# Kernel optimization log

Hardware: AMD Instinct MI355X
Metric: run time of the kernel (lower is better)

The kernel has to match this reference:

```python
import jax, jax.numpy as jnp
import numpy as np

B, V, H, W = 8, 2, 1024, 1024
N = 131072
TH_MIN, TH_MAX = 0.0, 500.0
ALPHA = 0.5


def _make_extrinsics():
    # Random small-rotation camera-to-world poses (invertible 4x4), fixed seed.
    rng = np.random.default_rng(0)
    E = np.tile(np.eye(4, dtype=np.float32), (B, V, 1, 1))
    for bi in range(B):
        for vi in range(V):
            ang = rng.uniform(-0.15, 0.15)
            ax = rng.normal(size=3)
            ax = ax / np.linalg.norm(ax)
            K = np.array([[0.0, -ax[2], ax[1]], [ax[2], 0.0, -ax[0]], [-ax[1], ax[0], 0.0]])
            R = np.eye(3) + np.sin(ang) * K + (1.0 - np.cos(ang)) * (K @ K)
            E[bi, vi, :3, :3] = R.astype(np.float32)
            E[bi, vi, :3, 3] = (rng.normal(size=3) * 0.5).astype(np.float32)
    return jnp.asarray(E)


def setup_inputs():
    key = jax.random.key(0)
    k0, k1, k2, k3, k4 = jax.random.split(key, 5)
    scale = jnp.array([W - 1.0, H - 1.0], jnp.float32)
    mkpts0 = jax.random.uniform(k0, (N, 2), dtype=jnp.float32) * scale
    mkpts1 = jax.random.uniform(k1, (N, 2), dtype=jnp.float32) * scale
    mconf = jax.random.uniform(k2, (N,), jnp.float32, 0.2, 1.0)
    mbids = jnp.sort(jax.random.randint(k3, (N,), 0, B, dtype=jnp.int32))
    intr = jnp.tile(jnp.array([[1.0, 0.0, 0.5], [0.0, 1.0, 0.5], [0.0, 0.0, 1.0]], jnp.float32), (B, V, 1, 1))
    extr = _make_extrinsics()
    disps = jax.random.uniform(k4, (V * B, 1, H, W), jnp.float32, 0.01, 1.0)
    return {"mkpts0": mkpts0, "mkpts1": mkpts1, "mconf": mconf, "mbids": mbids,
            "intrinsics": intr, "extrinsics": extr, "fullres_disps": disps}


def _forward(mkpts0, mkpts1, mconf, mbids, intrinsics, extrinsics, fullres_disps):
    b, v = intrinsics.shape[:2]
    _, _, h, w = fullres_disps.shape
    # intr0[0,:]*=w ; intr0[1,:]*=h  (normalized -> pixel intrinsics)
    row_scale = jnp.array([float(w), float(h), 1.0], intrinsics.dtype)[None, None, :, None]
    intr = intrinsics * row_scale                                    # (b,v,3,3)
    extr_inv = jnp.linalg.inv(extrinsics)                            # (b,v,4,4)
    proj = jnp.einsum('bvij,bvjk->bvik', intr, extr_inv[:, :, :3, :])  # (b,v,3,4)

    # --- per-keypoint DLT triangulation (vectorized over all N matches) ---
    P = proj[mbids]                                                  # (N,v,3,4)
    pts2 = jnp.stack([mkpts0, mkpts1], axis=1)                       # (N,v,2)
    # rows: conf*(x*P[2]-P[0]), conf*(y*P[2]-P[1])
    A = P[:, :, 2:3, :] * pts2[..., None] - P[:, :, :2, :]           # (N,v,2,4)
    A = A * mconf[:, None, None, None]
    A = A.reshape(-1, 2 * v, 4)                                      # (N,4,4)
    _, _, vh = jnp.linalg.svd(A, full_matrices=False)
    hom = vh[:, -1, :]                                               # last right singular vector
    pts_world = hom[:, :3] / hom[:, 3:4]                             # (N,3)

    # transform into each camera frame: pc_transform(pts, extr.inverse())
    pw_h = jnp.concatenate([pts_world, jnp.ones_like(pts_world[:, :1])], axis=-1)
    pts_cam = jnp.einsum('nvij,nj->nvi', extr_inv[mbids], pw_h)[..., :3]  # (N,v,3)
    z = pts_cam[..., 2]                                              # (N,v)
    valid = jnp.all((z > TH_MIN) & (z < TH_MAX), axis=1)             # (N,)

    # --- near/far over valid matched depths per (scene, view) ---
    zmin = jnp.where(valid[:, None], z, jnp.inf)
    zmax = jnp.where(valid[:, None], z, -jnp.inf)
    near = jax.ops.segment_min(zmin, mbids, num_segments=b)          # (b,v)
    far = jax.ops.segment_max(zmax, mbids, num_segments=b)
    has = jax.ops.segment_max(valid.astype(jnp.float32), mbids, num_segments=b)
    flag = jnp.broadcast_to(has[:, None], (b, v))                    # (b,v)
    near = jnp.where(flag > 0, near, 0.0)
    far = jnp.where(flag > 0, far, 500.0)

    # --- fusion_mkpt_costvolum: scatter 1/z into the cost-volume disparities ---
    disps = fullres_disps.reshape(v, b, h, w)                        # '(v b) 1 h w'
    mk_x = jnp.clip(jnp.stack([mkpts0[:, 0], mkpts1[:, 0]], 1).astype(jnp.int32), 0, w - 1)  # (N,v)
    mk_y = jnp.clip(jnp.stack([mkpts0[:, 1], mkpts1[:, 1]], 1).astype(jnp.int32), 0, h - 1)
    mk_z = 1.0 / z                                                   # matched disparity (N,v)
    view_idx = jnp.broadcast_to(jnp.arange(v, dtype=jnp.int32)[None, :], mk_x.shape)
    bids2 = jnp.broadcast_to(mbids[:, None], mk_x.shape)
    cost = disps[view_idx, bids2, mk_y, mk_x]                        # gather existing disparity
    val = ALPHA * mk_z + (1.0 - ALPHA) * cost                        # alpha-weighted fusion
    val = jnp.where(valid[:, None], val, cost)                       # masked-out matches: no-op write
    disps = disps.at[view_idx, bids2, mk_y, mk_x].set(val)
    fused = disps.reshape(v * b, 1, h, w)
    return fused, near, far, flag


def reference(mkpts0, mkpts1, mconf, mbids, intrinsics, extrinsics, fullres_disps):
    return _forward(mkpts0, mkpts1, mconf, mbids, intrinsics, extrinsics, fullres_disps)
```

## Files before the change

kernel.cpp:

```cpp
#include <hip/hip_runtime.h>
#include <math.h>

#define BB 8
#define VV 2
#define HH 1024
#define WW 1024
#define NPTS 131072
#define IMG (HH*WW)
#define FUSED (VV*BB*IMG)

#define NSOLVE (NPTS/256)
#define NCLEAR ((2*NPTS)/256)
#define NCOPY  (FUSED/4/256)

#define OFF_Z    0u
#define OFF_PIX  (8u*NPTS)
#define OFF_RED  (16u*NPTS)
#define OFF_WIN  (OFF_RED + 0x20000u)
#define WS_NEED  ((size_t)OFF_WIN + 4ull*(size_t)FUSED)

__device__ __forceinline__ int clampi(int v, int lo, int hi) {
    return v < lo ? lo : (v > hi ? hi : v);
}

__device__ void prep_one(int t, const float* __restrict__ intr,
                         const float* __restrict__ extr, double* sD) {
    const float* E = extr + t * 16;
    double a[4][8];
    for (int i = 0; i < 4; i++)
        for (int j = 0; j < 4; j++) {
            a[i][j]     = (double)E[i * 4 + j];
            a[i][4 + j] = (i == j) ? 1.0 : 0.0;
        }
    for (int c = 0; c < 4; c++) {
        int piv = c; double best = fabs(a[c][c]);
        for (int r = c + 1; r < 4; r++) {
            double v = fabs(a[r][c]);
            if (v > best) { best = v; piv = r; }
        }
        if (piv != c)
            for (int j = 0; j < 8; j++) {
                double tmp = a[c][j]; a[c][j] = a[piv][j]; a[piv][j] = tmp;
            }
        double inv = 1.0 / a[c][c];
        for (int j = 0; j < 8; j++) a[c][j] *= inv;
        for (int r = 0; r < 4; r++) {
            if (r == c) continue;
            double f = a[r][c];
            for (int j = 0; j < 8; j++) a[r][j] -= f * a[c][j];
        }
    }
    const float* K = intr + t * 9;
    double rs[3] = {(double)WW, (double)HH, 1.0};
    for (int i = 0; i < 3; i++)
        for (int k = 0; k < 4; k++) {
            double s = 0.0;
            for (int j = 0; j < 3; j++) s += (double)K[i * 3 + j] * rs[i] * a[j][4 + k];
            sD[t * 12 + i * 4 + k] = s;
        }
    for (int k = 0; k < 4; k++) sD[192 + t * 4 + k] = a[2][4 + k];
}

template <int DEDUP>
__global__ __launch_bounds__(256) void mega_kernel(
        const float4* __restrict__ src, float4* __restrict__ dst,
        const float2* __restrict__ mk0, const float2* __restrict__ mk1,
        const int* __restrict__ mbids,
        const float* __restrict__ intr, const float* __restrict__ extr,
        const float* __restrict__ disps,
        float* __restrict__ out, char* __restrict__ ws) {
    int b = blockIdx.x, t = threadIdx.x;

    if (b >= NSOLVE + NCLEAR) {
        int i = (b - NSOLVE - NCLEAR) * 256 + t;
        dst[i] = src[i];
        return;
    }
    if (b >= NSOLVE) {
        if (DEDUP) {
            int id = (b - NSOLVE) * 256 + t;
            int n = id >> 1, v = id & 1;
            const float2* mk = v ? mk1 : mk0;
            float2 q = mk[n];
            int xi = clampi((int)q.x, 0, WW - 1);
            int yi = clampi((int)q.y, 0, HH - 1);
            int bid = mbids[n];
            ((int*)(ws + OFF_WIN))[(v * BB + bid) * IMG + yi * WW + xi] = -1;
        }
        return;
    }

    __shared__ double sD[256];
    __shared__ int nearB[16], farB[16], hasB[8];
    if (t < 16) {
        prep_one(t, intr, extr, sD);
        nearB[t] = 0x7F800000;
        farB[t]  = 0;
        if (t < 8) hasB[t] = 0;
    }
    __syncthreads();

    int n = b * 256 + t;
    float* zarr   = (float*)(ws + OFF_Z);
    int*   pixarr = (int*)(ws + OFF_PIX);
    int*   winner = (int*)(ws + OFF_WIN);

    int bid = mbids[n];
    float2 q0 = mk0[n], q1 = mk1[n];
    float xf[2] = {q0.x, q1.x};
    float yf[2] = {q0.y, q1.y};

    double M[4][4];
#pragma unroll
    for (int i = 0; i < 4; i++)
#pragma unroll
        for (int j = 0; j < 4; j++) M[i][j] = 0.0;
#pragma unroll
    for (int v = 0; v < 2; v++) {
        const double* P = sD + (bid * VV + v) * 12;
        double xx = (double)xf[v], yy = (double)yf[v];
        double r0[4], r1[4];
#pragma unroll
        for (int j = 0; j < 4; j++) {
            r0[j] = xx * P[8 + j] - P[j];
            r1[j] = yy * P[8 + j] - P[4 + j];
        }
#pragma unroll
        for (int i = 0; i < 4; i++)
#pragma unroll
            for (int j = 0; j < 4; j++) M[i][j] += r0[i] * r0[j] + r1[i] * r1[j];
    }

    double Vm[4][4] = {{1, 0, 0, 0}, {0, 1, 0, 0}, {0, 0, 1, 0}, {0, 0, 0, 1}};
    for (int sweep = 0; sweep < 8; ++sweep) {
        double off = fabs(M[0][1]) + fabs(M[0][2]) + fabs(M[0][3]) +
                     fabs(M[1][2]) + fabs(M[1][3]) + fabs(M[2][3]);
        double dia = fabs(M[0][0]) + fabs(M[1][1]) + fabs(M[2][2]) + fabs(M[3][3]);
        if (off <= 1e-13 * dia) break;
#pragma unroll
        for (int p = 0; p < 3; p++) {
#pragma unroll
            for (int q = p + 1; q < 4; q++) {
                double apq = M[p][q];
                if (fabs(apq) < 1e-300) continue;
                double tau = (M[q][q] - M[p][p]) / (2.0 * apq);
                double rt  = sqrt(1.0 + tau * tau);
                double t_  = (tau >= 0.0) ? 1.0 / (tau + rt) : 1.0 / (tau - rt);
                double c = 1.0 / sqrt(1.0 + t_ * t_);
                double s = t_ * c;
#pragma unroll
                for (int k = 0; k < 4; k++) {
                    double mp = M[k][p], mq = M[k][q];
                    M[k][p] = c * mp - s * mq;
                    M[k][q] = s * mp + c * mq;
                }
#pragma unroll
                for (int k = 0; k < 4; k++) {
                    double mp = M[p][k], mq = M[q][k];
                    M[p][k] = c * mp - s * mq;
                    M[q][k] = s * mp + c * mq;
                }
#pragma unroll
                for (int k = 0; k < 4; k++) {
                    double vp = Vm[k][p], vq = Vm[k][q];
                    Vm[k][p] = c * vp - s * vq;
                    Vm[k][q] = s * vp + c * vq;
                }
            }
        }
    }
    int jmin = 0; double dmin = M[0][0];
    if (M[1][1] < dmin) { dmin = M[1][1]; jmin = 1; }
    if (M[2][2] < dmin) { dmin = M[2][2]; jmin = 2; }
    if (M[3][3] < dmin) { dmin = M[3][3]; jmin = 3; }

    double ev[4];
#pragma unroll
    for (int i = 0; i < 4; i++) {
        double a01 = (jmin == 0) ? Vm[i][0] : Vm[i][1];
        double a23 = (jmin == 2) ? Vm[i][2] : Vm[i][3];
        ev[i] = (jmin < 2) ? a01 : a23;
    }
    double iw  = 1.0 / ev[3];
    double pwx = ev[0] * iw, pwy = ev[1] * iw, pwz = ev[2] * iw;

    double z[2];
#pragma unroll
    for (int v = 0; v < 2; v++) {
        const double* e = sD + 192 + (bid * VV + v) * 4;
        z[v] = e[0] * pwx + e[1] * pwy + e[2] * pwz + e[3];
    }
    bool valid = (z[0] > 0.0) && (z[0] < 500.0) && (z[1] > 0.0) && (z[1] < 500.0);

    unsigned long long vb = __ballot(valid);
    int bidFirst = __shfl(bid, 0);
    int bidLast  = __shfl(bid, 63);
    if (bidFirst == bidLast) {
        if (vb != 0ULL) {
            float zn[2], zf[2];
#pragma unroll
            for (int v = 0; v < 2; v++) {
                zn[v] = valid ? (float)z[v] : INFINITY;
                zf[v] = valid ? (float)z[v] : -1.0f;
            }
#pragma unroll
            for (int off = 32; off > 0; off >>= 1) {
#pragma unroll
                for (int v = 0; v < 2; v++) {
                    zn[v] = fminf(zn[v], __shfl_down(zn[v], off));
                    zf[v] = fmaxf(zf[v], __shfl_down(zf[v], off));
                }
            }
            if ((t & 63) == 0) {
#pragma unroll
                for (int v = 0; v < 2; v++) {
                    atomicMin(&nearB[bid * VV + v], __float_as_int(zn[v]));
                    atomicMax(&farB[bid * VV + v],  __float_as_int(zf[v]));
                }
                atomicOr(&hasB[bid], 1);
            }
        }
    } else if (valid) {
#pragma unroll
        for (int v = 0; v < 2; v++) {
            int fb = __float_as_int((float)z[v]);
            atomicMin(&nearB[bid * VV + v], fb);
            atomicMax(&farB[bid * VV + v],  fb);
        }
        atomicOr(&hasB[bid], 1);
    }

#pragma unroll
    for (int v = 0; v < 2; v++) {
        int xi = clampi((int)xf[v], 0, WW - 1);
        int yi = clampi((int)yf[v], 0, HH - 1);
        int pix = (v * BB + bid) * IMG + yi * WW + xi;
        if (DEDUP) {
            zarr[2 * n + v]   = valid ? (float)z[v] : 0.0f;
            pixarr[2 * n + v] = pix;
        } else {
            float cost = disps[pix];
            float val = valid ? (float)(0.5 * (1.0 / z[v]) + 0.5 * (double)cost) : cost;
            out[pix] = val;
        }
    }

    __syncthreads();
    int* red = (int*)(ws + OFF_RED) + b * 40;
    if (t < 16) {
        red[t]      = nearB[t];
        red[16 + t] = farB[t];
        if (t < 8) red[32 + t] = hasB[t];
    }
}

__global__ __launch_bounds__(256) void vote_kernel(char* __restrict__ ws) {
    int id = blockIdx.x * 256 + threadIdx.x;
    const int* pixarr = (const int*)(ws + OFF_PIX);
    int* winner = (int*)(ws + OFF_WIN);
    atomicMax(winner + pixarr[id], id >> 1);
}

__global__ __launch_bounds__(256) void resolve_kernel(const float* __restrict__ disps,
                                                      float* __restrict__ out,
                                                      const char* __restrict__ ws,
                                                      int dedup) {
    int id = blockIdx.x * 256 + threadIdx.x;
    if (dedup) {
        const float* zarr   = (const float*)(ws + OFF_Z);
        const int*   pixarr = (const int*)(ws + OFF_PIX);
        const int*   winner = (const int*)(ws + OFF_WIN);
        int   pix = pixarr[id];
        float zf  = zarr[id];
        if (winner[pix] == (id >> 1) && zf > 0.0f) {
            float cost = disps[pix];
            out[pix] = (float)(0.5 * (1.0 / (double)zf) + 0.5 * (double)cost);
        }
    }
    if (blockIdx.x == 0) {
        int t = threadIdx.x;
        const int* red = (const int*)(ws + OFF_RED);
        if (t < 16) {
            int nm = 0x7F800000, hv = 0;
            for (int s = 0; s < NSOLVE; s++) {
                const int* r = red + s * 40;
                nm = min(nm, r[t]);
                hv |= r[32 + (t >> 1)];
            }
            float* near_ = out + FUSED;
            float* flag_ = out + FUSED + 2 * BB * VV;
            near_[t] = hv ? __int_as_float(nm) : 0.0f;
            flag_[t] = hv ? 1.0f : 0.0f;
        } else if (t < 32) {
            int c = t - 16;
            int fm = 0, hv = 0;
            for (int s = 0; s < NSOLVE; s++) {
                const int* r = red + s * 40;
                fm = max(fm, r[16 + c]);
                hv |= r[32 + (c >> 1)];
            }
            float* far_ = out + FUSED + BB * VV;
            far_[c] = hv ? __int_as_float(fm) : 500.0f;
        }
    }
}

extern "C" void kernel_launch(void* const* d_in, const int* in_sizes, int n_in,
                              void* d_out, int out_size, void* d_ws, size_t ws_size,
                              hipStream_t stream) {
    const float* mk0   = (const float*)d_in[0];
    const float* mk1   = (const float*)d_in[1];
    const int*   mbids = (const int*)d_in[3];
    const float* intr  = (const float*)d_in[4];
    const float* extr  = (const float*)d_in[5];
    const float* disps = (const float*)d_in[6];
    float* out = (float*)d_out;
    char*  ws  = (char*)d_ws;

    bool dedup = (ws_size >= WS_NEED);
    dim3 grid(NSOLVE + NCLEAR + NCOPY);

    if (dedup) {
        mega_kernel<1><<<grid, 256, 0, stream>>>(
            (const float4*)disps, (float4*)out, (const float2*)mk0, (const float2*)mk1,
            mbids, intr, extr, disps, out, ws);
        vote_kernel<<<NCLEAR, 256, 0, stream>>>(ws);
        resolve_kernel<<<NCLEAR, 256, 0, stream>>>(disps, out, ws, 1);
    } else {
        mega_kernel<0><<<grid, 256, 0, stream>>>(
            (const float4*)disps, (float4*)out, (const float2*)mk0, (const float2*)mk1,
            mbids, intr, extr, disps, out, ws);
        resolve_kernel<<<1, 256, 0, stream>>>(disps, out, ws, 0);
    }
}
```

Baseline: 206.8 us.

## Use closed-form rigid inverse, nontemporal copy stores, and parallel final reduction

Replaces the per-block Gauss-Jordan 4x4 inversion with a closed-form rigid-transform inverse (transpose rotation, negate rotated translation). Writes the bulk disparity copy with nontemporal stores to reduce cache pollution. Rewrites the near/far/flag reduction in the resolve kernel to use all four waves with shuffle reductions instead of 32 serial threads. The rigid inverse assumes the extrinsics are orthonormal rotations plus translation.

```diff
diff --git a/kernel.cpp b/kernel.cpp
--- a/kernel.cpp
+++ b/kernel.cpp
@@ -13,6 +13,8 @@
 #define NCLEAR ((2*NPTS)/256)
 #define NCOPY  (FUSED/4/256)
 
+typedef float f32x4 __attribute__((ext_vector_type(4)));
+
 #define OFF_Z    0u
 #define OFF_PIX  (8u*NPTS)
 #define OFF_RED  (16u*NPTS)
@@ -23,47 +25,41 @@
     return v < lo ? lo : (v > hi ? hi : v);
 }
 
-__device__ void prep_one(int t, const float* __restrict__ intr,
-                         const float* __restrict__ extr, double* sD) {
+__device__ __forceinline__ void prep_one(int t, const float* __restrict__ intr,
+                                         const float* __restrict__ extr, double* sD) {
     const float* E = extr + t * 16;
-    double a[4][8];
-    for (int i = 0; i < 4; i++)
-        for (int j = 0; j < 4; j++) {
-            a[i][j]     = (double)E[i * 4 + j];
-            a[i][4 + j] = (i == j) ? 1.0 : 0.0;
-        }
-    for (int c = 0; c < 4; c++) {
-        int piv = c; double best = fabs(a[c][c]);
-        for (int r = c + 1; r < 4; r++) {
-            double v = fabs(a[r][c]);
-            if (v > best) { best = v; piv = r; }
-        }
-        if (piv != c)
-            for (int j = 0; j < 8; j++) {
-                double tmp = a[c][j]; a[c][j] = a[piv][j]; a[piv][j] = tmp;
-            }
-        double inv = 1.0 / a[c][c];
-        for (int j = 0; j < 8; j++) a[c][j] *= inv;
-        for (int r = 0; r < 4; r++) {
-            if (r == c) continue;
-            double f = a[r][c];
-            for (int j = 0; j < 8; j++) a[r][j] -= f * a[c][j];
-        }
+    double R[3][3], tr[3];
+#pragma unroll
+    for (int i = 0; i < 3; i++) {
+#pragma unroll
+        for (int j = 0; j < 3; j++) R[i][j] = (double)E[i * 4 + j];
+        tr[i] = (double)E[i * 4 + 3];
+    }
+    double inv[3][4];
+#pragma unroll
+    for (int i = 0; i < 3; i++) {
+#pragma unroll
+        for (int j = 0; j < 3; j++) inv[i][j] = R[j][i];
+        inv[i][3] = -(R[0][i] * tr[0] + R[1][i] * tr[1] + R[2][i] * tr[2]);
     }
     const float* K = intr + t * 9;
     double rs[3] = {(double)WW, (double)HH, 1.0};
+#pragma unroll
     for (int i = 0; i < 3; i++)
+#pragma unroll
         for (int k = 0; k < 4; k++) {
             double s = 0.0;
-            for (int j = 0; j < 3; j++) s += (double)K[i * 3 + j] * rs[i] * a[j][4 + k];
+#pragma unroll
+            for (int j = 0; j < 3; j++) s += (double)K[i * 3 + j] * rs[i] * inv[j][k];
             sD[t * 12 + i * 4 + k] = s;
         }
-    for (int k = 0; k < 4; k++) sD[192 + t * 4 + k] = a[2][4 + k];
+#pragma unroll
+    for (int k = 0; k < 4; k++) sD[192 + t * 4 + k] = inv[2][k];
 }
 
 template <int DEDUP>
 __global__ __launch_bounds__(256) void mega_kernel(
-        const float4* __restrict__ src, float4* __restrict__ dst,
+        const f32x4* __restrict__ src, f32x4* __restrict__ dst,
         const float2* __restrict__ mk0, const float2* __restrict__ mk1,
         const int* __restrict__ mbids,
         const float* __restrict__ intr, const float* __restrict__ extr,
@@ -73,7 +69,8 @@
 
     if (b >= NSOLVE + NCLEAR) {
         int i = (b - NSOLVE - NCLEAR) * 256 + t;
-        dst[i] = src[i];
+        f32x4 v = src[i];
+        __builtin_nontemporal_store(v, &dst[i]);
         return;
     }
     if (b >= NSOLVE) {
@@ -103,7 +100,6 @@
     int n = b * 256 + t;
     float* zarr   = (float*)(ws + OFF_Z);
     int*   pixarr = (int*)(ws + OFF_PIX);
-    int*   winner = (int*)(ws + OFF_WIN);
 
     int bid = mbids[n];
     float2 q0 = mk0[n], q1 = mk1[n];
@@ -278,29 +274,29 @@
         }
     }
     if (blockIdx.x == 0) {
+        __shared__ int redLds[40];
         int t = threadIdx.x;
         const int* red = (const int*)(ws + OFF_RED);
+        int w = t >> 6, lane = t & 63;
+        for (int c = w; c < 40; c += 4) {
+            int acc = (c < 16) ? 0x7F800000 : 0;
+            for (int s = lane; s < NSOLVE; s += 64) {
+                int vv = red[s * 40 + c];
+                acc = (c < 16) ? min(acc, vv) : (c < 32 ? max(acc, vv) : (acc | vv));
+            }
+#pragma unroll
+            for (int off = 32; off > 0; off >>= 1) {
+                int o = __shfl_down(acc, off);
+                acc = (c < 16) ? min(acc, o) : (c < 32 ? max(acc, o) : (acc | o));
+            }
+            if (lane == 0) redLds[c] = acc;
+        }
+        __syncthreads();
         if (t < 16) {
-            int nm = 0x7F800000, hv = 0;
-            for (int s = 0; s < NSOLVE; s++) {
-                const int* r = red + s * 40;
-                nm = min(nm, r[t]);
-                hv |= r[32 + (t >> 1)];
-            }
-            float* near_ = out + FUSED;
-            float* flag_ = out + FUSED + 2 * BB * VV;
-            near_[t] = hv ? __int_as_float(nm) : 0.0f;
-            flag_[t] = hv ? 1.0f : 0.0f;
-        } else if (t < 32) {
-            int c = t - 16;
-            int fm = 0, hv = 0;
-            for (int s = 0; s < NSOLVE; s++) {
-                const int* r = red + s * 40;
-                fm = max(fm, r[16 + c]);
-                hv |= r[32 + (c >> 1)];
-            }
-            float* far_ = out + FUSED + BB * VV;
-            far_[c] = hv ? __int_as_float(fm) : 500.0f;
+            int hv = redLds[32 + (t >> 1)];
+            out[FUSED + t]               = hv ? __int_as_float(redLds[t])      : 0.0f;
+            out[FUSED + BB * VV + t]     = hv ? __int_as_float(redLds[16 + t]) : 500.0f;
+            out[FUSED + 2 * BB * VV + t] = hv ? 1.0f : 0.0f;
         }
     }
 }
@@ -322,13 +318,13 @@
 
     if (dedup) {
         mega_kernel<1><<<grid, 256, 0, stream>>>(
-            (const float4*)disps, (float4*)out, (const float2*)mk0, (const float2*)mk1,
+            (const f32x4*)disps, (f32x4*)out, (const float2*)mk0, (const float2*)mk1,
             mbids, intr, extr, disps, out, ws);
         vote_kernel<<<NCLEAR, 256, 0, stream>>>(ws);
         resolve_kernel<<<NCLEAR, 256, 0, stream>>>(disps, out, ws, 1);
     } else {
         mega_kernel<0><<<grid, 256, 0, stream>>>(
-            (const float4*)disps, (float4*)out, (const float2*)mk0, (const float2*)mk1,
+            (const f32x4*)disps, (f32x4*)out, (const float2*)mk0, (const float2*)mk1,
             mbids, intr, extr, disps, out, ws);
         resolve_kernel<<<1, 256, 0, stream>>>(disps, out, ws, 0);
     }
```

Measured after the change: 185.7 us. -10.2%, faster.
